# Kernel tuning notes

Measured on AMD Instinct MI355X. Metric: run time of the kernel, lower is better.

The kernel has to match this reference:

```python
import jax, jax.numpy as jnp
import numpy as np

V, D, H, O = 32000, 256, 512, 6
B, T = 128, 2048


def setup_inputs() -> dict:
    key = jax.random.key(0)
    ks = jax.random.split(key, 8)
    s = lambda k, shp, fan: jax.random.normal(k, shp, jnp.float32) / np.float32(np.sqrt(fan))
    return dict(
        token_ids=jax.random.randint(ks[0], (B, T), 0, V),
        emb=s(ks[1], (V, D), D),
        gru_wih=s(ks[2], (3 * H, D), D),
        gru_whh=s(ks[3], (3 * H, H), H),
        gru_b=jnp.zeros((3 * H,), jnp.float32),
        gru_bn=jnp.zeros((H,), jnp.float32),
        lstm_wih=s(ks[4], (4 * H, H), H),
        lstm_whh=s(ks[5], (4 * H, H), H),
        lstm_b=jnp.zeros((4 * H,), jnp.float32),
        head_w=s(ks[6], (O, H), H),
        head_b=jnp.zeros((O,), jnp.float32),
    )


def reference(token_ids, emb, gru_wih, gru_whh, gru_b, gru_bn,
              lstm_wih, lstm_whh, lstm_b, head_w, head_b):
    x = emb[token_ids]                      # (B, T, D) embedding lookup
    xs = jnp.swapaxes(x, 0, 1)              # (T, B, D) for scan over time
    h = gru_whh.shape[1]
    h0 = jnp.zeros((x.shape[0], h), x.dtype)

    def step(carry, xt):
        hg, hl, cl = carry
        # --- equinox GRUCell ---
        ig = xt @ gru_wih.T + gru_b         # (B, 3H)
        hh = hg @ gru_whh.T                 # (B, 3H)
        ir, iz, inn = jnp.split(ig, 3, axis=-1)
        hr, hz, hn = jnp.split(hh, 3, axis=-1)
        r = jax.nn.sigmoid(ir + hr)
        z = jax.nn.sigmoid(iz + hz)
        n = jnp.tanh(inn + r * (hn + gru_bn))
        hg_new = n + z * (hg - n)           # == (1-z)*n + z*hg
        # --- equinox LSTMCell (input = GRU output) ---
        lin = hg_new @ lstm_wih.T + hl @ lstm_whh.T + lstm_b  # (B, 4H)
        i_, f_, g_, o_ = jnp.split(lin, 4, axis=-1)
        c_new = jax.nn.sigmoid(f_) * cl + jax.nn.sigmoid(i_) * jnp.tanh(g_)
        h_new = jax.nn.sigmoid(o_) * jnp.tanh(c_new)
        return (hg_new, h_new, c_new), None

    (_, h_final, _), _ = jax.lax.scan(step, (h0, h0, h0), xs)
    return h_final @ head_w.T + head_b      # (B, O)
```

## Files before the change

### kernel.cpp

```cpp
#include <hip/hip_runtime.h>
#include <hip/hip_bf16.h>


typedef short v8s __attribute__((ext_vector_type(8)));
typedef float v4f __attribute__((ext_vector_type(4)));
typedef unsigned long long u64;

#define T_STEPS 2048
#define RING_OFF 8192
#define DYN_LDS 150816

#define MFMA16(a, b, c) __builtin_amdgcn_mfma_f32_16x16x32_bf16((a), (b), (c), 0, 0, 0)

__device__ __forceinline__ v4f v4zero() { v4f z = {0.f, 0.f, 0.f, 0.f}; return z; }
__device__ __forceinline__ float sigf(float x) { return 1.f / (1.f + __expf(-x)); }
__device__ __forceinline__ float tanhf_fast(float x) { return 1.f - 2.f / (1.f + __expf(2.f * x)); }

__device__ __forceinline__ ushort f2us(float v) {
  __hip_bfloat16 b = __float2bfloat16(v);
  return *reinterpret_cast<ushort*>(&b);
}
__device__ __forceinline__ float us2f(ushort u) {
  __hip_bfloat16 b;
  *reinterpret_cast<ushort*>(&b) = u;
  return __bfloat162float(b);
}
__device__ __forceinline__ void cvt_hilo(float v, ushort& h, ushort& l) {
  __hip_bfloat16 bh = __float2bfloat16(v);
  float r = v - __bfloat162float(bh);
  __hip_bfloat16 bl = __float2bfloat16(r);
  h = *reinterpret_cast<ushort*>(&bh);
  l = *reinterpret_cast<ushort*>(&bl);
}
__device__ __forceinline__ void stage4(ushort* hi, ushort* lo, const float* src) {
  float4 v = *(const float4*)src;
  float a[4] = {v.x, v.y, v.z, v.w};
#pragma unroll
  for (int j = 0; j < 4; ++j) { ushort h, l; cvt_hilo(a[j], h, l); hi[j] = h; lo[j] = l; }
}
__device__ __forceinline__ void stage4h(ushort* hi, const float* src) {
  float4 v = *(const float4*)src;
  float a[4] = {v.x, v.y, v.z, v.w};
#pragma unroll
  for (int j = 0; j < 4; ++j) hi[j] = f2us(a[j]);
}
__device__ __forceinline__ void st_wt(ushort* p, ushort v) {
  __hip_atomic_store(p, v, __ATOMIC_RELAXED, __HIP_MEMORY_SCOPE_AGENT);
}
__device__ __forceinline__ v8s ld_a16(const ushort* p) {
  u64 a = __hip_atomic_load((const u64*)p, __ATOMIC_RELAXED, __HIP_MEMORY_SCOPE_AGENT);
  u64 b = __hip_atomic_load((const u64*)p + 1, __ATOMIC_RELAXED, __HIP_MEMORY_SCOPE_AGENT);
  union { u64 u[2]; v8s v; } r;
  r.u[0] = a; r.u[1] = b;
  return r.v;
}

__device__ __forceinline__ int poll_ge(const int* p, int tgt, long& budget) {
  while (budget > 0) {
    if (__hip_atomic_load(p, __ATOMIC_RELAXED, __HIP_MEMORY_SCOPE_AGENT) >= tgt) return 1;
    __builtin_amdgcn_s_sleep(1);
    --budget;
  }
  return 0;
}
__device__ __forceinline__ int poll4_ge(const int* base, int tgt, long& budget) {
  while (budget > 0) {
    int s = __hip_atomic_load(base,       __ATOMIC_RELAXED, __HIP_MEMORY_SCOPE_AGENT)
          + __hip_atomic_load(base +  64, __ATOMIC_RELAXED, __HIP_MEMORY_SCOPE_AGENT)
          + __hip_atomic_load(base + 128, __ATOMIC_RELAXED, __HIP_MEMORY_SCOPE_AGENT)
          + __hip_atomic_load(base + 192, __ATOMIC_RELAXED, __HIP_MEMORY_SCOPE_AGENT);
    if (s >= tgt) return 1;
    __builtin_amdgcn_s_sleep(1);
    --budget;
  }
  return 0;
}

__global__ void __launch_bounds__(256, 1) rnn_persistent(
    const int* __restrict__ tok,
    const float* __restrict__ emb,
    const float* __restrict__ gwih,
    const float* __restrict__ gwhh,
    const float* __restrict__ gb,
    const float* __restrict__ gbn,
    const float* __restrict__ lwih,
    const float* __restrict__ lwhh,
    const float* __restrict__ lb,
    char* __restrict__ ws,
    int hstride, int has_lo)
{
  extern __shared__ char smem[];
  const int tid  = threadIdx.x;
  const int wgid = blockIdx.x;
  const bool is_gru = (wgid < 64);
  const int sub = is_gru ? wgid : (wgid - 64);
  const int bg  = sub & 1;
  const int cg  = sub >> 1;
  const int colbase = cg * 16;
  const int b0 = bg * 64;
  const int stripe = cg & 3;
  const int lane = tid & 63;
  const int wave = tid >> 6;
  const int quad = lane >> 4;
  const int r16  = lane & 15;

  int* cnt = (int*)ws;
  int* gru_done  = cnt + bg * 256;
  int* lstm_done = cnt + 512 + bg * 256;
  int* boot      = cnt + 1024;
  ushort* ring = (ushort*)(ws + RING_OFF);
  const int slotE = 128 * hstride;
  ushort* hlb = ring + 2 * slotE;

  const int mrow  = wave * 16 + r16;
  const int bglob = b0 + wave * 16 + quad * 4;
  const int col   = colbase + r16;
  long budget = 3000000;

  if (is_gru) {
    ushort* smemU = (ushort*)smem;
    const int WIH_HI = 0, WIH_LO = 12672, WHH_HI = 25344, WHH_LO = 50304;
    int* okf = (int*)(smem + 150528);

    for (int i = tid; i < 48 * 64; i += 256) {
      int row = i >> 6, q = (i & 63) * 4;
      int gate = row >> 4, c = colbase + (row & 15);
      stage4(&smemU[WIH_HI + row * 264 + q], &smemU[WIH_LO + row * 264 + q],
             gwih + (long)(gate * 512 + c) * 256 + q);
    }
    for (int i = tid; i < 48 * 128; i += 256) {
      int row = i >> 7, k = (i & 127) * 4;
      int gate = row >> 4, c = colbase + (row & 15);
      stage4(&smemU[WHH_HI + row * 520 + k], &smemU[WHH_LO + row * 520 + k],
             gwhh + (long)(gate * 512 + c) * 512 + k);
    }
    const float b_r  = gb[col];
    const float b_z  = gb[512 + col];
    const float b_in = gb[1024 + col];
    const float bnv  = gbn[col];
    __syncthreads();

    if (tid == 0) {
      __hip_atomic_fetch_add(boot, 1, __ATOMIC_RELEASE, __HIP_MEMORY_SCOPE_AGENT);
      long bb = 3000000;
      okf[0] = poll_ge(boot, 128, bb);
    }
    __syncthreads();
    if (!okf[0]) { if (wgid == 0 && tid == 0) st_wt(&hlb[slotE + 0], f2us(1.0e4f)); return; }

    v4f acc_r, acc_z, acc_nx;
    float hgreg[4] = {0.f, 0.f, 0.f, 0.f};
    float4 xa[16];

    auto prefetch_x = [&](int tn) {
      int ntok = tok[(b0 + mrow) * T_STEPS + tn];
      const float* xrow = emb + (long)ntok * 256;
#pragma unroll
      for (int kk = 0; kk < 8; ++kk) {
        xa[2 * kk]     = *(const float4*)(xrow + kk * 32 + quad * 8);
        xa[2 * kk + 1] = *(const float4*)(xrow + kk * 32 + quad * 8 + 4);
      }
    };
    auto accx_compute = [&]() {
      acc_r = v4zero(); acc_z = v4zero(); acc_nx = v4zero();
#pragma unroll
      for (int kk = 0; kk < 8; ++kk) {
        float xv[8] = {xa[2 * kk].x, xa[2 * kk].y, xa[2 * kk].z, xa[2 * kk].w,
                       xa[2 * kk + 1].x, xa[2 * kk + 1].y, xa[2 * kk + 1].z, xa[2 * kk + 1].w};
        v8s ahi, alo;
#pragma unroll
        for (int j = 0; j < 8; ++j) { ushort h, l; cvt_hilo(xv[j], h, l); ahi[j] = (short)h; alo[j] = (short)l; }
        const int orr = (r16) * 264 + kk * 32 + quad * 8;
        const int oz  = (16 + r16) * 264 + kk * 32 + quad * 8;
        const int on  = (32 + r16) * 264 + kk * 32 + quad * 8;
        v8s brh = *(const v8s*)&smemU[WIH_HI + orr], brl = *(const v8s*)&smemU[WIH_LO + orr];
        v8s bzh = *(const v8s*)&smemU[WIH_HI + oz],  bzl = *(const v8s*)&smemU[WIH_LO + oz];
        v8s bnh = *(const v8s*)&smemU[WIH_HI + on],  bnl = *(const v8s*)&smemU[WIH_LO + on];
        acc_r = MFMA16(ahi, brh, acc_r); acc_r = MFMA16(alo, brh, acc_r); acc_r = MFMA16(ahi, brl, acc_r);
        acc_z = MFMA16(ahi, bzh, acc_z); acc_z = MFMA16(alo, bzh, acc_z); acc_z = MFMA16(ahi, bzl, acc_z);
        acc_nx = MFMA16(ahi, bnh, acc_nx); acc_nx = MFMA16(alo, bnh, acc_nx); acc_nx = MFMA16(ahi, bnl, acc_nx);
      }
    };

    prefetch_x(0);
    accx_compute();

    for (int t = 0; t < T_STEPS; ++t) {
      if (tid == 0) {
        int ok = poll4_ge(gru_done, 32 * t, budget);
        if (ok) ok = poll4_ge(lstm_done, 32 * (t - 1), budget);
        okf[0] = ok;
      }
      __syncthreads();
      if (!okf[0]) { if (tid == 0) st_wt(&hlb[slotE + 2 + wgid], f2us(100.f)); break; }

      v8s ahi[16], alo[16];
      if (t > 0) {
        const ushort* hrow = ring + ((t - 1) & 1) * slotE + (b0 + mrow) * hstride;
#pragma unroll
        for (int kk = 0; kk < 16; ++kk) {
          ahi[kk] = ld_a16(&hrow[kk * 32 + quad * 8]);
          if (has_lo) alo[kk] = ld_a16(&hrow[512 + kk * 32 + quad * 8]);
        }
      }
      if (t + 1 < T_STEPS) prefetch_x(t + 1);

      v4f acc_nh = v4zero();
      if (t > 0) {
#pragma unroll
        for (int kk = 0; kk < 16; ++kk) {
          const int orr = (r16) * 520 + kk * 32 + quad * 8;
          const int oz  = (16 + r16) * 520 + kk * 32 + quad * 8;
          const int on  = (32 + r16) * 520 + kk * 32 + quad * 8;
          v8s brh = *(const v8s*)&smemU[WHH_HI + orr], brl = *(const v8s*)&smemU[WHH_LO + orr];
          v8s bzh = *(const v8s*)&smemU[WHH_HI + oz],  bzl = *(const v8s*)&smemU[WHH_LO + oz];
          v8s bnh = *(const v8s*)&smemU[WHH_HI + on],  bnl = *(const v8s*)&smemU[WHH_LO + on];
          acc_r = MFMA16(ahi[kk], brh, acc_r); acc_r = MFMA16(ahi[kk], brl, acc_r);
          acc_z = MFMA16(ahi[kk], bzh, acc_z); acc_z = MFMA16(ahi[kk], bzl, acc_z);
          acc_nh = MFMA16(ahi[kk], bnh, acc_nh); acc_nh = MFMA16(ahi[kk], bnl, acc_nh);
          if (has_lo) {
            acc_r = MFMA16(alo[kk], brh, acc_r);
            acc_z = MFMA16(alo[kk], bzh, acc_z);
            acc_nh = MFMA16(alo[kk], bnh, acc_nh);
          }
        }
      }

      ushort* slotT = ring + (t & 1) * slotE;
#pragma unroll
      for (int rg = 0; rg < 4; ++rg) {
        float r = sigf(acc_r[rg] + b_r);
        float z = sigf(acc_z[rg] + b_z);
        float nn = tanhf_fast(acc_nx[rg] + b_in + r * (acc_nh[rg] + bnv));
        float hnew = nn + z * (hgreg[rg] - nn);
        hgreg[rg] = hnew;
        ushort uh = f2us(hnew);
        const int rb = (bglob + rg) * hstride;
        st_wt(&slotT[rb + col], uh);
        if (has_lo) st_wt(&slotT[rb + 512 + col], f2us(hnew - us2f(uh)));
      }

      __syncthreads();
      if (tid == 0)
        __hip_atomic_fetch_add(gru_done + stripe * 64, 1, __ATOMIC_RELAXED, __HIP_MEMORY_SCOPE_AGENT);
      if (t + 1 < T_STEPS) accx_compute();
    }
  } else {
    ushort* smemU = (ushort*)smem;
    int* okf = (int*)(smem + 132096);

    for (int i = tid; i < 64 * 256; i += 256) {
      int row = i >> 8, k = (i & 255) * 4;
      int gate = row >> 4, c = colbase + (row & 15);
      long grow = gate * 512 + c;
      const float* src = (k < 512) ? (lwih + grow * 512 + k) : (lwhh + grow * 512 + (k - 512));
      stage4h(&smemU[row * 1032 + k], src);
    }
    const float b_i = lb[col];
    const float b_f = lb[512 + col];
    const float b_g = lb[1024 + col];
    const float b_o = lb[1536 + col];
    __syncthreads();

    if (tid == 0) {
      __hip_atomic_fetch_add(boot, 1, __ATOMIC_RELEASE, __HIP_MEMORY_SCOPE_AGENT);
      long bb = 3000000;
      okf[0] = poll_ge(boot, 128, bb);
    }
    __syncthreads();
    if (!okf[0]) { if (wgid == 64 && tid == 0) st_wt(&hlb[slotE + 1], f2us(1.0e4f)); return; }

    float creg[4] = {0.f, 0.f, 0.f, 0.f};

    for (int t = 0; t < T_STEPS; ++t) {
      if (tid == 0) {
        int ok = poll4_ge(gru_done, 32 * (t + 1), budget);
        if (ok) ok = poll4_ge(lstm_done, 32 * t, budget);
        okf[0] = ok;
      }
      __syncthreads();
      if (!okf[0]) { if (tid == 0) st_wt(&hlb[slotE + 2 + wgid], f2us(100.f)); break; }

      v8s ghi[16], glo[16];
      {
        const ushort* hrow = ring + (t & 1) * slotE + (b0 + mrow) * hstride;
#pragma unroll
        for (int kk = 0; kk < 16; ++kk) {
          ghi[kk] = ld_a16(&hrow[kk * 32 + quad * 8]);
          if (has_lo) glo[kk] = ld_a16(&hrow[512 + kk * 32 + quad * 8]);
        }
      }
      v8s lhi[16], llo[16];
      const ushort* lrow = hlb + ((t - 1) & 1) * slotE + (b0 + mrow) * hstride;
      if (t > 0) {
#pragma unroll
        for (int kk = 0; kk < 16; ++kk) lhi[kk] = ld_a16(&lrow[kk * 32 + quad * 8]);
      }

      v4f ai = v4zero(), af = v4zero(), ag = v4zero(), ao = v4zero();
#pragma unroll
      for (int kk = 0; kk < 16; ++kk) {
        v8s bi = *(const v8s*)&smemU[(r16) * 1032 + kk * 32 + quad * 8];
        v8s bf = *(const v8s*)&smemU[(16 + r16) * 1032 + kk * 32 + quad * 8];
        v8s bgv = *(const v8s*)&smemU[(32 + r16) * 1032 + kk * 32 + quad * 8];
        v8s bo = *(const v8s*)&smemU[(48 + r16) * 1032 + kk * 32 + quad * 8];
        ai = MFMA16(ghi[kk], bi, ai); af = MFMA16(ghi[kk], bf, af);
        ag = MFMA16(ghi[kk], bgv, ag); ao = MFMA16(ghi[kk], bo, ao);
        if (has_lo) {
          ai = MFMA16(glo[kk], bi, ai); af = MFMA16(glo[kk], bf, af);
          ag = MFMA16(glo[kk], bgv, ag); ao = MFMA16(glo[kk], bo, ao);
        }
      }

      if (t > 0) {
        if (has_lo) {
#pragma unroll
          for (int kk = 0; kk < 16; ++kk) llo[kk] = ld_a16(&lrow[512 + kk * 32 + quad * 8]);
        }
#pragma unroll
        for (int kk = 0; kk < 16; ++kk) {
          v8s bi = *(const v8s*)&smemU[(r16) * 1032 + 512 + kk * 32 + quad * 8];
          v8s bf = *(const v8s*)&smemU[(16 + r16) * 1032 + 512 + kk * 32 + quad * 8];
          v8s bgv = *(const v8s*)&smemU[(32 + r16) * 1032 + 512 + kk * 32 + quad * 8];
          v8s bo = *(const v8s*)&smemU[(48 + r16) * 1032 + 512 + kk * 32 + quad * 8];
          ai = MFMA16(lhi[kk], bi, ai); af = MFMA16(lhi[kk], bf, af);
          ag = MFMA16(lhi[kk], bgv, ag); ao = MFMA16(lhi[kk], bo, ao);
        }
        if (has_lo) {
#pragma unroll
          for (int kk = 0; kk < 16; ++kk) {
            v8s bi = *(const v8s*)&smemU[(r16) * 1032 + 512 + kk * 32 + quad * 8];
            v8s bf = *(const v8s*)&smemU[(16 + r16) * 1032 + 512 + kk * 32 + quad * 8];
            v8s bgv = *(const v8s*)&smemU[(32 + r16) * 1032 + 512 + kk * 32 + quad * 8];
            v8s bo = *(const v8s*)&smemU[(48 + r16) * 1032 + 512 + kk * 32 + quad * 8];
            ai = MFMA16(llo[kk], bi, ai); af = MFMA16(llo[kk], bf, af);
            ag = MFMA16(llo[kk], bgv, ag); ao = MFMA16(llo[kk], bo, ao);
          }
        }
      }

      ushort* hout = hlb + (t & 1) * slotE;
#pragma unroll
      for (int rg = 0; rg < 4; ++rg) {
        float i_ = sigf(ai[rg] + b_i), f_ = sigf(af[rg] + b_f);
        float g_ = tanhf_fast(ag[rg] + b_g), o_ = sigf(ao[rg] + b_o);
        float cn = f_ * creg[rg] + i_ * g_;
        creg[rg] = cn;
        float hv = o_ * tanhf_fast(cn);
        ushort uh = f2us(hv);
        const int rb = (bglob + rg) * hstride;
        st_wt(&hout[rb + col], uh);
        if (has_lo) st_wt(&hout[rb + 512 + col], f2us(hv - us2f(uh)));
      }

      __syncthreads();
      if (tid == 0)
        __hip_atomic_fetch_add(lstm_done + stripe * 64, 1, __ATOMIC_RELAXED, __HIP_MEMORY_SCOPE_AGENT);
    }
  }
}

__global__ void head_kernel(const char* __restrict__ ws,
                            const float* __restrict__ hw,
                            const float* __restrict__ hbias,
                            float* __restrict__ out,
                            int hstride, int has_lo) {
  const ushort* h1 = (const ushort*)(ws + RING_OFF) + 3 * 128 * hstride;
  const int b = blockIdx.x, l = threadIdx.x;
  const int k0 = l * 8;
  v8s hi = ld_a16(&h1[b * hstride + k0]);
  v8s lo;
  if (has_lo) lo = ld_a16(&h1[b * hstride + 512 + k0]);
  float acc[6] = {0.f, 0.f, 0.f, 0.f, 0.f, 0.f};
#pragma unroll
  for (int j = 0; j < 8; ++j) {
    float h = us2f((ushort)hi[j]);
    if (has_lo) h += us2f((ushort)lo[j]);
#pragma unroll
    for (int o = 0; o < 6; ++o) acc[o] += h * hw[o * 512 + k0 + j];
  }
#pragma unroll
  for (int o = 0; o < 6; ++o) {
    float v = acc[o];
    for (int off = 32; off > 0; off >>= 1) v += __shfl_down(v, off);
    if (l == 0) out[b * 6 + o] = v + hbias[o];
  }
}

__global__ void init_ws(int* cnt) {
  int i = blockIdx.x * blockDim.x + threadIdx.x;
  if (i < 2048)
    __hip_atomic_store(cnt + i, 0, __ATOMIC_RELAXED, __HIP_MEMORY_SCOPE_AGENT);
}

__global__ void ws_too_small_marker(float* out) {
  if (threadIdx.x == 0 && blockIdx.x == 0) out[0] = 12345.0f;
}

extern "C" void kernel_launch(void* const* d_in, const int* in_sizes, int n_in,
                              void* d_out, int out_size, void* d_ws, size_t ws_size,
                              hipStream_t stream) {
  const int*   tok  = (const int*)d_in[0];
  const float* emb  = (const float*)d_in[1];
  const float* gwih = (const float*)d_in[2];
  const float* gwhh = (const float*)d_in[3];
  const float* gb   = (const float*)d_in[4];
  const float* gbn  = (const float*)d_in[5];
  const float* lwih = (const float*)d_in[6];
  const float* lwhh = (const float*)d_in[7];
  const float* lb   = (const float*)d_in[8];
  const float* hw   = (const float*)d_in[9];
  const float* hb   = (const float*)d_in[10];

  (void)in_sizes; (void)n_in; (void)out_size;

  const size_t WS_A = (size_t)RING_OFF + 4ull * 128 * 1024 * 2;
  const size_t WS_B = (size_t)RING_OFF + 4ull * 128 * 512 * 2;
  if (ws_size < WS_B) {
    hipLaunchKernelGGL(ws_too_small_marker, dim3(1), dim3(64), 0, stream, (float*)d_out);
    return;
  }
  const int has_lo  = (ws_size >= (size_t)WS_A) ? 1 : 0;
  const int hstride = has_lo ? 1024 : 512;

  (void)hipFuncSetAttribute(reinterpret_cast<const void*>(rnn_persistent),
                            hipFuncAttributeMaxDynamicSharedMemorySize, DYN_LDS);
  hipLaunchKernelGGL(init_ws, dim3(8), dim3(256), 0, stream, (int*)d_ws);
  hipLaunchKernelGGL(rnn_persistent, dim3(128), dim3(256), DYN_LDS, stream,
                     tok, emb, gwih, gwhh, gb, gbn, lwih, lwhh, lb,
                     (char*)d_ws, hstride, has_lo);
  hipLaunchKernelGGL(head_kernel, dim3(128), dim3(64), 0, stream,
                     (const char*)d_ws, hw, hb, (float*)d_out, hstride, has_lo);
}
```

Before: 33.13 ms.

## Replace workgroup barrier polling with per-wave fused flag polling and release counters

Each wave now polls the GRU and LSTM progress counters itself: the lanes of a wave split the loads across eight counter slots and reduce them with shuffles. Each wave then bumps its own counter with release semantics, replacing the thread-0 poll plus two __syncthreads per step. This removes workgroup barriers from the per-timestep critical path of the persistent recurrent kernel and lets waves proceed independently. The risks are more counter traffic, since every wave polls, and subtle memory-ordering or count-target errors. Targets change to 128 per step (32 WGs times 4 waves), and the GRU t=0 wait is skipped.

```diff
diff --git a/kernel.cpp b/kernel.cpp
--- a/kernel.cpp
+++ b/kernel.cpp
@@ -63,13 +63,19 @@
   }
   return 0;
 }
-__device__ __forceinline__ int poll4_ge(const int* base, int tgt, long& budget) {
+__device__ __forceinline__ int poll2_fused(const int* baseA, int tgtA,
+                                           const int* baseB, int tgtB,
+                                           int lane, long& budget) {
+  const int w = lane & 7;
+  const int* p = (((lane >> 3) & 1) ? baseB : baseA) + w * 32;
   while (budget > 0) {
-    int s = __hip_atomic_load(base,       __ATOMIC_RELAXED, __HIP_MEMORY_SCOPE_AGENT)
-          + __hip_atomic_load(base +  64, __ATOMIC_RELAXED, __HIP_MEMORY_SCOPE_AGENT)
-          + __hip_atomic_load(base + 128, __ATOMIC_RELAXED, __HIP_MEMORY_SCOPE_AGENT)
-          + __hip_atomic_load(base + 192, __ATOMIC_RELAXED, __HIP_MEMORY_SCOPE_AGENT);
-    if (s >= tgt) return 1;
+    int v = __hip_atomic_load(p, __ATOMIC_RELAXED, __HIP_MEMORY_SCOPE_AGENT);
+    v += __shfl_xor(v, 1);
+    v += __shfl_xor(v, 2);
+    v += __shfl_xor(v, 4);
+    int sa = __shfl(v, 0);
+    int sb = __shfl(v, 8);
+    if (sa >= tgtA && sb >= tgtB) return 1;
     __builtin_amdgcn_s_sleep(1);
     --budget;
   }
@@ -98,11 +104,11 @@
   const int cg  = sub >> 1;
   const int colbase = cg * 16;
   const int b0 = bg * 64;
-  const int stripe = cg & 3;
   const int lane = tid & 63;
   const int wave = tid >> 6;
   const int quad = lane >> 4;
   const int r16  = lane & 15;
+  const int swrd = ((cg & 1) << 2) | wave;
 
   int* cnt = (int*)ws;
   int* gru_done  = cnt + bg * 256;
@@ -186,13 +192,12 @@
     accx_compute();
 
     for (int t = 0; t < T_STEPS; ++t) {
-      if (tid == 0) {
-        int ok = poll4_ge(gru_done, 32 * t, budget);
-        if (ok) ok = poll4_ge(lstm_done, 32 * (t - 1), budget);
-        okf[0] = ok;
-      }
-      __syncthreads();
-      if (!okf[0]) { if (tid == 0) st_wt(&hlb[slotE + 2 + wgid], f2us(100.f)); break; }
+      if (t > 0) {
+        if (!poll2_fused(gru_done, 128 * t, lstm_done, 128 * (t - 1), lane, budget)) {
+          if (lane == 0) st_wt(&hlb[slotE + 2 + wgid], f2us(100.f));
+          break;
+        }
+      }
 
       v8s ahi[16], alo[16];
       if (t > 0) {
@@ -240,9 +245,8 @@
         if (has_lo) st_wt(&slotT[rb + 512 + col], f2us(hnew - us2f(uh)));
       }
 
-      __syncthreads();
-      if (tid == 0)
-        __hip_atomic_fetch_add(gru_done + stripe * 64, 1, __ATOMIC_RELAXED, __HIP_MEMORY_SCOPE_AGENT);
+      if (lane == 0)
+        __hip_atomic_fetch_add(gru_done + swrd * 32, 1, __ATOMIC_RELEASE, __HIP_MEMORY_SCOPE_AGENT);
       if (t + 1 < T_STEPS) accx_compute();
     }
   } else {
@@ -273,13 +277,10 @@
     float creg[4] = {0.f, 0.f, 0.f, 0.f};
 
     for (int t = 0; t < T_STEPS; ++t) {
-      if (tid == 0) {
-        int ok = poll4_ge(gru_done, 32 * (t + 1), budget);
-        if (ok) ok = poll4_ge(lstm_done, 32 * t, budget);
-        okf[0] = ok;
-      }
-      __syncthreads();
-      if (!okf[0]) { if (tid == 0) st_wt(&hlb[slotE + 2 + wgid], f2us(100.f)); break; }
+      if (!poll2_fused(gru_done, 128 * (t + 1), lstm_done, 128 * t, lane, budget)) {
+        if (lane == 0) st_wt(&hlb[slotE + 2 + wgid], f2us(100.f));
+        break;
+      }
 
       v8s ghi[16], glo[16];
       {
@@ -353,9 +354,8 @@
         if (has_lo) st_wt(&hout[rb + 512 + col], f2us(hv - us2f(uh)));
       }
 
-      __syncthreads();
-      if (tid == 0)
-        __hip_atomic_fetch_add(lstm_done + stripe * 64, 1, __ATOMIC_RELAXED, __HIP_MEMORY_SCOPE_AGENT);
+      if (lane == 0)
+        __hip_atomic_fetch_add(lstm_done + swrd * 32, 1, __ATOMIC_RELEASE, __HIP_MEMORY_SCOPE_AGENT);
     }
   }
 }
```

Measured after the change: 55.13 ms. 1.66x slower.

## Parallelize flag polling across lanes and pack hidden-state stores into 64-bit writes

Applied to the files above, without the earlier changes.

Replaces the single-thread serial polling of eight progress counters with a wave-0 poll in which eight lanes each load one counter and combine the results with shuffles. It also skips the poll at t=0 in the GRU path and moves the x prefetch ahead of the wait. Hidden-state writes are packed with lane shuffles so each group of four lanes issues one 64-bit atomic store instead of four 16-bit stores. Together these aim to cut per-step synchronization latency and store traffic in the persistent recurrence, at the cost of extra shuffles and a dependence on the r16 lane layout matching contiguous columns.

```diff
diff --git a/kernel.cpp b/kernel.cpp
--- a/kernel.cpp
+++ b/kernel.cpp
@@ -47,6 +47,16 @@
 __device__ __forceinline__ void st_wt(ushort* p, ushort v) {
   __hip_atomic_store(p, v, __ATOMIC_RELAXED, __HIP_MEMORY_SCOPE_AGENT);
 }
+__device__ __forceinline__ void st_row32(ushort* rowp, int r16, ushort uh) {
+  unsigned v32 = (unsigned)uh;
+  unsigned nb = (unsigned)__shfl_xor((int)v32, 1);
+  if (!(r16 & 1)) v32 |= (nb << 16);
+  unsigned hi32 = (unsigned)__shfl_xor((int)v32, 2);
+  if ((r16 & 3) == 0) {
+    u64 v = (u64)v32 | ((u64)hi32 << 32);
+    __hip_atomic_store((u64*)(rowp + r16), v, __ATOMIC_RELAXED, __HIP_MEMORY_SCOPE_AGENT);
+  }
+}
 __device__ __forceinline__ v8s ld_a16(const ushort* p) {
   u64 a = __hip_atomic_load((const u64*)p, __ATOMIC_RELAXED, __HIP_MEMORY_SCOPE_AGENT);
   u64 b = __hip_atomic_load((const u64*)p + 1, __ATOMIC_RELAXED, __HIP_MEMORY_SCOPE_AGENT);
@@ -63,13 +73,20 @@
   }
   return 0;
 }
-__device__ __forceinline__ int poll4_ge(const int* base, int tgt, long& budget) {
+__device__ __forceinline__ int poll2_w0(const int* gbase, int tgtA,
+                                        const int* lbase, int tgtB,
+                                        int lane, long& budget) {
+  const int* p = gbase;
+  if (lane >= 4 && lane < 8) p = lbase + (lane - 4) * 64;
+  else if (lane < 4) p = gbase + lane * 64;
   while (budget > 0) {
-    int s = __hip_atomic_load(base,       __ATOMIC_RELAXED, __HIP_MEMORY_SCOPE_AGENT)
-          + __hip_atomic_load(base +  64, __ATOMIC_RELAXED, __HIP_MEMORY_SCOPE_AGENT)
-          + __hip_atomic_load(base + 128, __ATOMIC_RELAXED, __HIP_MEMORY_SCOPE_AGENT)
-          + __hip_atomic_load(base + 192, __ATOMIC_RELAXED, __HIP_MEMORY_SCOPE_AGENT);
-    if (s >= tgt) return 1;
+    int v = 0;
+    if (lane < 8) v = __hip_atomic_load(p, __ATOMIC_RELAXED, __HIP_MEMORY_SCOPE_AGENT);
+    v += __shfl_xor(v, 1);
+    v += __shfl_xor(v, 2);
+    int sa = __shfl(v, 0);
+    int sb = __shfl(v, 4);
+    if (sa >= tgtA && sb >= tgtB) return 1;
     __builtin_amdgcn_s_sleep(1);
     --budget;
   }
@@ -186,13 +203,16 @@
     accx_compute();
 
     for (int t = 0; t < T_STEPS; ++t) {
-      if (tid == 0) {
-        int ok = poll4_ge(gru_done, 32 * t, budget);
-        if (ok) ok = poll4_ge(lstm_done, 32 * (t - 1), budget);
-        okf[0] = ok;
-      }
-      __syncthreads();
-      if (!okf[0]) { if (tid == 0) st_wt(&hlb[slotE + 2 + wgid], f2us(100.f)); break; }
+      if (t + 1 < T_STEPS) prefetch_x(t + 1);
+
+      if (t > 0) {
+        if (wave == 0) {
+          int ok = poll2_w0(gru_done, 32 * t, lstm_done, 32 * (t - 1), lane, budget);
+          if (lane == 0) okf[0] = ok;
+        }
+        __syncthreads();
+        if (!okf[0]) { if (tid == 0) st_wt(&hlb[slotE + 2 + wgid], f2us(100.f)); break; }
+      }
 
       v8s ahi[16], alo[16];
       if (t > 0) {
@@ -203,7 +223,6 @@
           if (has_lo) alo[kk] = ld_a16(&hrow[512 + kk * 32 + quad * 8]);
         }
       }
-      if (t + 1 < T_STEPS) prefetch_x(t + 1);
 
       v4f acc_nh = v4zero();
       if (t > 0) {
@@ -235,9 +254,9 @@
         float hnew = nn + z * (hgreg[rg] - nn);
         hgreg[rg] = hnew;
         ushort uh = f2us(hnew);
-        const int rb = (bglob + rg) * hstride;
-        st_wt(&slotT[rb + col], uh);
-        if (has_lo) st_wt(&slotT[rb + 512 + col], f2us(hnew - us2f(uh)));
+        ushort* rp = &slotT[(bglob + rg) * hstride + colbase];
+        st_row32(rp, r16, uh);
+        if (has_lo) st_row32(rp + 512, r16, f2us(hnew - us2f(uh)));
       }
 
       __syncthreads();
@@ -273,10 +292,9 @@
     float creg[4] = {0.f, 0.f, 0.f, 0.f};
 
     for (int t = 0; t < T_STEPS; ++t) {
-      if (tid == 0) {
-        int ok = poll4_ge(gru_done, 32 * (t + 1), budget);
-        if (ok) ok = poll4_ge(lstm_done, 32 * t, budget);
-        okf[0] = ok;
+      if (wave == 0) {
+        int ok = poll2_w0(gru_done, 32 * (t + 1), lstm_done, 32 * t, lane, budget);
+        if (lane == 0) okf[0] = ok;
       }
       __syncthreads();
       if (!okf[0]) { if (tid == 0) st_wt(&hlb[slotE + 2 + wgid], f2us(100.f)); break; }
@@ -348,9 +366,9 @@
         creg[rg] = cn;
         float hv = o_ * tanhf_fast(cn);
         ushort uh = f2us(hv);
-        const int rb = (bglob + rg) * hstride;
-        st_wt(&hout[rb + col], uh);
-        if (has_lo) st_wt(&hout[rb + 512 + col], f2us(hv - us2f(uh)));
+        ushort* rp = &hout[(bglob + rg) * hstride + colbase];
+        st_row32(rp, r16, uh);
+        if (has_lo) st_row32(rp + 512, r16, f2us(hv - us2f(uh)));
       }
 
       __syncthreads();
```

New measurement: 35.15 ms. +6.1%, slower.
